# Kernel tuning notes

Hardware: AMD Instinct MI355X
Metric: run time of the kernel (lower is better)

Reference implementation:

```python
import jax, jax.numpy as jnp
import numpy as np

N_NODES = 50000
N_EDGES = 800000
IN_DIM = 64
OUT_DIM = 64
EDGE_DIM = 16
LN_EPS = 1e-5


def setup_inputs() -> dict:
    key = jax.random.key(0)
    ks = jax.random.split(key, 12)
    def lin(k, fan_in, fan_out):
        # torch nn.Linear default init: U(-1/sqrt(fan_in), 1/sqrt(fan_in))
        kw, kb = jax.random.split(k)
        bound = 1.0 / np.sqrt(fan_in)
        W = jax.random.uniform(kw, (fan_in, fan_out), jnp.float32, -bound, bound)
        b = jax.random.uniform(kb, (fan_out,), jnp.float32, -bound, bound)
        return W, b
    x = jax.random.normal(ks[0], (N_NODES, IN_DIM), jnp.float32)
    edge_index = jax.random.randint(ks[1], (2, N_EDGES), 0, N_NODES, jnp.int64 if jax.config.jax_enable_x64 else jnp.int32)
    edge_features = jax.random.normal(ks[2], (N_EDGES, EDGE_DIM), jnp.float32)
    W1, b1 = lin(ks[3], IN_DIM + EDGE_DIM, OUT_DIM)   # msg_mlp layer 1
    W2, b2 = lin(ks[4], OUT_DIM, OUT_DIM)             # msg_mlp layer 2
    W3, b3 = lin(ks[5], IN_DIM + OUT_DIM, OUT_DIM)    # update_mlp
    gamma = jnp.ones((OUT_DIM,), jnp.float32)
    beta = jnp.zeros((OUT_DIM,), jnp.float32)
    return {"x": x, "edge_index": edge_index, "edge_features": edge_features,
            "W1": W1, "b1": b1, "W2": W2, "b2": b2, "W3": W3, "b3": b3,
            "gamma": gamma, "beta": beta}


def reference(x, edge_index, edge_features, W1, b1, W2, b2, W3, b3, gamma, beta):
    num_nodes = x.shape[0]
    src, dst = edge_index[0], edge_index[1]
    # gather source node feats, concat with edge feats -> message MLP
    msg_in = jnp.concatenate([x[src], edge_features], axis=-1)           # [E, in+edge]
    h = jax.nn.relu(msg_in @ W1 + b1)
    messages = h @ W2 + b2                                               # [E, out]
    # scatter-add aggregate + mean by in-degree (count + 1e-8)
    agg = jax.ops.segment_sum(messages, dst, num_segments=num_nodes)     # [N, out]
    cnt = jax.ops.segment_sum(jnp.ones((messages.shape[0],), x.dtype), dst,
                              num_segments=num_nodes)[:, None]           # [N, 1]
    agg = agg / (cnt + 1e-8)
    # update MLP + residual (Identity since in_dim == out_dim) + LayerNorm
    updated = jax.nn.relu(jnp.concatenate([x, agg], axis=-1) @ W3 + b3)  # [N, out]
    y = updated + x
    mu = jnp.mean(y, axis=-1, keepdims=True)
    var = jnp.var(y, axis=-1, keepdims=True)
    return (y - mu) * jax.lax.rsqrt(var + LN_EPS) * gamma + beta
```

## Files before the change

### kernel.cpp

```cpp
#include <hip/hip_runtime.h>

typedef unsigned short u16;
typedef unsigned int u32;
typedef short short8 __attribute__((ext_vector_type(8)));
typedef short short4v __attribute__((ext_vector_type(4)));
typedef float floatx4 __attribute__((ext_vector_type(4)));

#define NE 800000
#define NNODES 50000
#define NBLK 196

#define EDGE_GRID 1536

#define LDS_FENCE() __asm__ volatile("s_waitcnt lgkmcnt(0)" ::: "memory")

__device__ __forceinline__ u16 f2bf(float f) {
    u32 r;
    asm("v_cvt_pk_bf16_f32 %0, %1, %2" : "=v"(r) : "v"(f), "v"(f));
    return (u16)r;
}
__device__ __forceinline__ u32 f2bf2(float lo, float hi) {
    u32 r;
    asm("v_cvt_pk_bf16_f32 %0, %1, %2" : "=v"(r) : "v"(lo), "v"(hi));
    return r;
}
__device__ __forceinline__ float bf2f(u16 u) {
    union { unsigned int i; float f; } v; v.i = ((unsigned int)u) << 16; return v.f;
}
__device__ __forceinline__ short8 pack8(const float4 a, const float4 b) {
    union { short8 s; u32 u[4]; } o;
    o.u[0] = f2bf2(a.x, a.y);
    o.u[1] = f2bf2(a.z, a.w);
    o.u[2] = f2bf2(b.x, b.y);
    o.u[3] = f2bf2(b.z, b.w);
    return o.s;
}
__device__ __forceinline__ short8 ld8_bf(const float* __restrict__ p) {
    return pack8(*(const float4*)p, *(const float4*)(p + 4));
}

#define MFMA16(a, b, c) __builtin_amdgcn_mfma_f32_16x16x32_bf16(a, b, c, 0, 0, 0)

__global__ __launch_bounds__(256) void prep_kernel(
    const float* __restrict__ x, const int* __restrict__ ei,
    int* __restrict__ hist, u16* __restrict__ xbf, float* __restrict__ agg)
{
    const int id = blockIdx.x * 256 + threadIdx.x;
    if (id < NE) {
        atomicAdd(&hist[ei[NE + id]], 1);
        float4 z; z.x = 0.f; z.y = 0.f; z.z = 0.f; z.w = 0.f;
        *(float4*)&agg[(size_t)id * 4] = z;
    }
    if (id < NNODES * 8) {
        *(short8*)&xbf[(size_t)id * 8] = ld8_bf(x + (size_t)id * 8);
    }
}

__global__ __launch_bounds__(256) void scan1_kernel(
    const int* __restrict__ hist, int* __restrict__ cursor, int* __restrict__ bsum)
{
    const int i = blockIdx.x * 256 + threadIdx.x;
    const int lane = threadIdx.x & 63;
    const int w = threadIdx.x >> 6;
    const int v = (i < NNODES) ? hist[i] : 0;
    int inc = v;
    #pragma unroll
    for (int o = 1; o < 64; o <<= 1) {
        const int tt = __shfl_up(inc, o);
        if (lane >= o) inc += tt;
    }
    __shared__ int ws[4];
    if (lane == 63) ws[w] = inc;
    __syncthreads();
    int add = 0;
    for (int j = 0; j < w; ++j) add += ws[j];
    const int excl = inc - v + add;
    if (i < NNODES) cursor[i] = excl;
    if (threadIdx.x == 255) bsum[blockIdx.x] = excl + v;
}

__global__ __launch_bounds__(256) void scatter_kernel(
    const int* __restrict__ ei, int* __restrict__ cursor,
    const int* __restrict__ bsum, uint2* __restrict__ sde)
{
    __shared__ int bsx[256];
    __shared__ int ws[4];
    {
        const int tid = threadIdx.x;
        const int lane = tid & 63;
        const int w = tid >> 6;
        const int v = (tid < NBLK) ? bsum[tid] : 0;
        int inc = v;
        #pragma unroll
        for (int o = 1; o < 64; o <<= 1) {
            const int tt = __shfl_up(inc, o);
            if (lane >= o) inc += tt;
        }
        if (lane == 63) ws[w] = inc;
        __syncthreads();
        int add = 0;
        for (int j = 0; j < w; ++j) add += ws[j];
        bsx[tid] = inc - v + add;
    }
    __syncthreads();

    const int e = blockIdx.x * 256 + threadIdx.x;
    if (e < NE) {
        const int dst = ei[NE + e];
        const int p = atomicAdd(&cursor[dst], 1) + bsx[dst >> 8];
        uint2 v;
        v.x = (u32)e;
        v.y = ((u32)ei[e] << 16) | (u32)dst;
        sde[p] = v;
    }
}

__global__ __launch_bounds__(256) void edge_kernel(
    const u16* __restrict__ xbf, const float* __restrict__ ef,
    const float* __restrict__ w1, const float* __restrict__ b1,
    const float* __restrict__ w2, const float* __restrict__ b2,
    const uint2* __restrict__ sde, float* __restrict__ agg)
{
    constexpr int S1 = 104;
    __shared__ u16 A1[4][16 * S1];
    __shared__ int Ds[4][16];
    __shared__ u16 W2f[2][4][64 * 8];

    const int wid  = threadIdx.x >> 6;
    const int lane = threadIdx.x & 63;
    const int q    = lane >> 4;
    const int c    = lane & 15;
    const int r4   = lane >> 2;
    const int p4   = lane & 3;

    short8 w1f[3][4];
    #pragma unroll
    for (int kk = 0; kk < 3; ++kk)
        #pragma unroll
        for (int nn = 0; nn < 4; ++nn)
            #pragma unroll
            for (int j = 0; j < 8; ++j) {
                const int k = kk * 32 + q * 8 + j;
                w1f[kk][nn][j] = (k < 80) ? (short)f2bf(w1[k * 64 + nn * 16 + c]) : (short)0;
            }
    if (wid == 0) {
        #pragma unroll
        for (int kk = 0; kk < 2; ++kk)
            #pragma unroll
            for (int nn = 0; nn < 4; ++nn) {
                short8 f;
                #pragma unroll
                for (int j = 0; j < 8; ++j) {
                    const int k = kk * 32 + q * 8 + j;
                    f[j] = (short)f2bf(w2[k * 64 + nn * 16 + c]);
                }
                *(short8*)&W2f[kk][nn][lane * 8] = f;
            }
    }
    float b1v[4], b2v[4];
    #pragma unroll
    for (int nn = 0; nn < 4; ++nn) {
        b1v[nn] = b1[nn * 16 + c];
        b2v[nn] = b2[nn * 16 + c];
    }
    if (q == 1) {
        const short8 z8 = {0, 0, 0, 0, 0, 0, 0, 0};
        *(short8*)&A1[wid][c * S1 + 80] = z8;
        *(short8*)&A1[wid][c * S1 + 88] = z8;
    }
    __syncthreads();

    const floatx4 zero = {0.f, 0.f, 0.f, 0.f};
    const int ntile = NE / 16;
    const int stride = gridDim.x * 4;
    int t = blockIdx.x * 4 + wid;

    uint2 sdB; u32 eB;
    short8 xa, xb; float4 ev;
    int dcur;
    {
        const uint2 sdA = sde[t * 16 + c];
        const u32  eA  = sde[t * 16 + r4].x;
        dcur = (int)(sdA.y & 0xffffu);
        const int sA = (int)(sdA.y >> 16);
        int tb = t + stride; if (tb >= ntile) tb = ntile - 1;
        sdB = sde[tb * 16 + c];
        eB  = sde[tb * 16 + r4].x;
        const u16* xp = xbf + (size_t)sA * 64 + q * 16;
        xa = *(const short8*)xp;
        xb = *(const short8*)(xp + 8);
        ev = *(const float4*)(ef + (size_t)eA * 16 + p4 * 4);
    }

    for (; t < ntile; t += stride) {
        u16* arow = &A1[wid][c * S1 + q * 16];
        *(short8*)arow       = xa;
        *(short8*)(arow + 8) = xb;
        {
            union { short4v s; u32 u[2]; } e4;
            e4.u[0] = f2bf2(ev.x, ev.y);
            e4.u[1] = f2bf2(ev.z, ev.w);
            *(short4v*)&A1[wid][r4 * S1 + 64 + p4 * 4] = e4.s;
        }
        if (q == 0) Ds[wid][c] = dcur;
        LDS_FENCE();

        short8 a1k[3];
        #pragma unroll
        for (int kk = 0; kk < 3; ++kk)
            a1k[kk] = *(const short8*)&A1[wid][c * S1 + kk * 32 + q * 8];

        const int dnext = (int)(sdB.y & 0xffffu);
        {
            const int sN = (int)(sdB.y >> 16);
            const u16* xp = xbf + (size_t)sN * 64 + q * 16;
            xa = *(const short8*)xp;
            xb = *(const short8*)(xp + 8);
            ev = *(const float4*)(ef + (size_t)eB * 16 + p4 * 4);
        }
        {
            int tb = t + 2 * stride; if (tb >= ntile) tb = ntile - 1;
            sdB = sde[tb * 16 + c];
            eB  = sde[tb * 16 + r4].x;
        }

        #pragma unroll
        for (int nn = 0; nn < 4; ++nn) {
            floatx4 acc = MFMA16(a1k[0], w1f[0][nn], zero);
            acc = MFMA16(a1k[1], w1f[1][nn], acc);
            acc = MFMA16(a1k[2], w1f[2][nn], acc);
            #pragma unroll
            for (int r = 0; r < 4; ++r) {
                const float h = fmaxf(acc[r] + b1v[nn], 0.f);
                A1[wid][(q * 4 + r) * S1 + nn * 16 + c] = f2bf(h);
            }
        }
        LDS_FENCE();

        short8 a2k[2];
        #pragma unroll
        for (int kk = 0; kk < 2; ++kk)
            a2k[kk] = *(const short8*)&A1[wid][c * S1 + kk * 32 + q * 8];

        #pragma unroll
        for (int nn = 0; nn < 4; ++nn) {
            const short8 wf0 = *(const short8*)&W2f[0][nn][lane * 8];
            const short8 wf1 = *(const short8*)&W2f[1][nn][lane * 8];
            floatx4 mg = MFMA16(a2k[0], wf0, zero);
            mg = MFMA16(a2k[1], wf1, mg);
            #pragma unroll
            for (int r = 0; r < 4; ++r)
                A1[wid][(q * 4 + r) * S1 + nn * 16 + c] = f2bf(mg[r] + b2v[nn]);
        }
        LDS_FENCE();

        int dc = Ds[wid][0];
        float acc = bf2f(A1[wid][lane]);
        #pragma unroll
        for (int row = 1; row < 16; ++row) {
            const int d = Ds[wid][row];
            const float v = bf2f(A1[wid][row * S1 + lane]);
            if (d == dc) {
                acc += v;
            } else {
                atomicAdd(&agg[(size_t)dc * 64 + lane], acc);
                dc = d;
                acc = v;
            }
        }
        atomicAdd(&agg[(size_t)dc * 64 + lane], acc);

        LDS_FENCE();

        dcur = dnext;
    }
}

__global__ __launch_bounds__(256) void node_kernel(
    const u16* __restrict__ xbf, const float* __restrict__ w3,
    const float* __restrict__ b3, const float* __restrict__ g,
    const float* __restrict__ bb, const float* __restrict__ agg,
    const int* __restrict__ hist, float* __restrict__ out)
{
    constexpr int S3 = 136;
    __shared__ u16 Cs[4][16 * S3];

    const int wid  = threadIdx.x >> 6;
    const int lane = threadIdx.x & 63;
    const int q    = lane >> 4;
    const int c    = lane & 15;

    short8 w3f[4][4];
    #pragma unroll
    for (int kk = 0; kk < 4; ++kk)
        #pragma unroll
        for (int nn = 0; nn < 4; ++nn)
            #pragma unroll
            for (int j = 0; j < 8; ++j) {
                const int k = kk * 32 + q * 8 + j;
                w3f[kk][nn][j] = (short)f2bf(w3[k * 64 + nn * 16 + c]);
            }
    float b3v[4], gv[4], bv[4];
    #pragma unroll
    for (int nn = 0; nn < 4; ++nn) {
        b3v[nn] = b3[nn * 16 + c];
        gv[nn]  = g[nn * 16 + c];
        bv[nn]  = bb[nn * 16 + c];
    }

    const floatx4 zero = {0.f, 0.f, 0.f, 0.f};
    const int ntile = NNODES / 16;

    for (int t = blockIdx.x * 4 + wid; t < ntile; t += gridDim.x * 4) {
        const int n0 = t * 16;
        const int node = n0 + c;
        u16* crow = &Cs[wid][c * S3];

        if (q < 2) {
            const u16* xp = xbf + (size_t)node * 64 + q * 32;
            *(short8*)&crow[q * 32]      = *(const short8*)xp;
            *(short8*)&crow[q * 32 + 8]  = *(const short8*)(xp + 8);
            *(short8*)&crow[q * 32 + 16] = *(const short8*)(xp + 16);
            *(short8*)&crow[q * 32 + 24] = *(const short8*)(xp + 24);
        } else {
            const int p = q - 2;
            const float inv = 1.0f / ((float)hist[node] + 1e-8f);
            const float* ap = agg + (size_t)node * 64 + p * 32;
            #pragma unroll
            for (int gi = 0; gi < 4; ++gi) {
                const float4 v0 = *(const float4*)(ap + gi * 8);
                const float4 v1 = *(const float4*)(ap + gi * 8 + 4);
                union { short8 s; u32 u[4]; } o;
                o.u[0] = f2bf2(v0.x * inv, v0.y * inv);
                o.u[1] = f2bf2(v0.z * inv, v0.w * inv);
                o.u[2] = f2bf2(v1.x * inv, v1.y * inv);
                o.u[3] = f2bf2(v1.z * inv, v1.w * inv);
                *(short8*)&crow[64 + p * 32 + gi * 8] = o.s;
            }
        }
        LDS_FENCE();

        short8 af[4];
        #pragma unroll
        for (int kk = 0; kk < 4; ++kk)
            af[kk] = *(const short8*)&Cs[wid][c * S3 + kk * 32 + q * 8];

        float y[4][4];
        float s[4]  = {0.f, 0.f, 0.f, 0.f};
        float ss[4] = {0.f, 0.f, 0.f, 0.f};
        #pragma unroll
        for (int nn = 0; nn < 4; ++nn) {
            floatx4 acc = MFMA16(af[0], w3f[0][nn], zero);
            acc = MFMA16(af[1], w3f[1][nn], acc);
            acc = MFMA16(af[2], w3f[2][nn], acc);
            acc = MFMA16(af[3], w3f[3][nn], acc);
            #pragma unroll
            for (int r = 0; r < 4; ++r) {
                const float upd = fmaxf(acc[r] + b3v[nn], 0.f);
                const float xv = bf2f(Cs[wid][(q * 4 + r) * S3 + nn * 16 + c]);
                const float yy = upd + xv;
                y[r][nn] = yy;
                s[r] += yy;
                ss[r] += yy * yy;
            }
        }

        #pragma unroll
        for (int r = 0; r < 4; ++r) {
            float sr = s[r], sq = ss[r];
            #pragma unroll
            for (int off = 1; off < 16; off <<= 1) {
                sr += __shfl_xor(sr, off);
                sq += __shfl_xor(sq, off);
            }
            const float mu  = sr * (1.0f / 64.0f);
            const float var = sq * (1.0f / 64.0f) - mu * mu;
            const float rs  = rsqrtf(var + 1e-5f);
            float* op = out + (size_t)(n0 + q * 4 + r) * 64 + c;
            #pragma unroll
            for (int nn = 0; nn < 4; ++nn)
                op[nn * 16] = (y[r][nn] - mu) * rs * gv[nn] + bv[nn];
        }
    }
}

extern "C" void kernel_launch(void* const* d_in, const int* in_sizes, int n_in,
                              void* d_out, int out_size, void* d_ws, size_t ws_size,
                              hipStream_t stream) {
    const float* x   = (const float*)d_in[0];
    const int*   ei  = (const int*)d_in[1];
    const float* ef  = (const float*)d_in[2];
    const float* w1  = (const float*)d_in[3];
    const float* b1  = (const float*)d_in[4];
    const float* w2  = (const float*)d_in[5];
    const float* b2  = (const float*)d_in[6];
    const float* w3  = (const float*)d_in[7];
    const float* b3  = (const float*)d_in[8];
    const float* g   = (const float*)d_in[9];
    const float* bb  = (const float*)d_in[10];

    float* agg   = (float*)d_ws;
    int* hist    = (int*)d_ws + 3200000;
    int* cursor  = hist + NNODES;
    int* bsum    = cursor + NNODES;
    int* bsumx   = bsum + 256;
    u16* xbf     = (u16*)(bsumx + 256);
    uint2* sde   = (uint2*)((int*)d_ws + 4900512);

    hipMemsetAsync(hist, 0, (size_t)NNODES * sizeof(int), stream);
    prep_kernel<<<3125, 256, 0, stream>>>(x, ei, hist, xbf, agg);
    scan1_kernel<<<NBLK, 256, 0, stream>>>(hist, cursor, bsum);
    scatter_kernel<<<3125, 256, 0, stream>>>(ei, cursor, bsum, sde);
    edge_kernel<<<EDGE_GRID, 256, 0, stream>>>(xbf, ef, w1, b1, w2, b2, sde, agg);
    node_kernel<<<782, 256, 0, stream>>>(xbf, w3, b3, g, bb, agg, hist, (float*)d_out);
}
```

Before: 274.7 us.

## Use atomic work counter for dynamic edge-tile scheduling across waves

Replaces the static grid-stride assignment of 16-edge tiles in the edge kernel with a global atomic counter. Each wave claims its next tile one iteration ahead, which is meant to balance uneven tile costs such as atomic scatter runs. The memset is widened so the counter starts at zero. The bf16 conversion also moves from the packed hardware instruction to a software round-to-nearest-even, and the edge-feature packing now uses the scalar helper. The costs are one extra same-address atomic per tile per wave, which can contend across all waves, and more ALU work per conversion.

```diff
diff --git a/kernel.cpp b/kernel.cpp
--- a/kernel.cpp
+++ b/kernel.cpp
@@ -15,9 +15,8 @@
 #define LDS_FENCE() __asm__ volatile("s_waitcnt lgkmcnt(0)" ::: "memory")
 
 __device__ __forceinline__ u16 f2bf(float f) {
-    u32 r;
-    asm("v_cvt_pk_bf16_f32 %0, %1, %2" : "=v"(r) : "v"(f), "v"(f));
-    return (u16)r;
+    union { float f; unsigned int i; } v; v.f = f;
+    return (u16)((v.i + 0x7fffu + ((v.i >> 16) & 1u)) >> 16);
 }
 __device__ __forceinline__ u32 f2bf2(float lo, float hi) {
     u32 r;
@@ -119,7 +118,8 @@
     const u16* __restrict__ xbf, const float* __restrict__ ef,
     const float* __restrict__ w1, const float* __restrict__ b1,
     const float* __restrict__ w2, const float* __restrict__ b2,
-    const uint2* __restrict__ sde, float* __restrict__ agg)
+    const uint2* __restrict__ sde, float* __restrict__ agg,
+    int* __restrict__ ctr)
 {
     constexpr int S1 = 104;
     __shared__ u16 A1[4][16 * S1];
@@ -172,18 +172,28 @@
 
     const floatx4 zero = {0.f, 0.f, 0.f, 0.f};
     const int ntile = NE / 16;
-    const int stride = gridDim.x * 4;
-    int t = blockIdx.x * 4 + wid;
+
+    int t_cur, t_nxt;
+    {
+        int v0 = 0, v1 = 0;
+        if (lane == 0) {
+            v0 = atomicAdd(ctr, 1);
+            v1 = atomicAdd(ctr, 1);
+        }
+        t_cur = __shfl(v0, 0);
+        t_nxt = __shfl(v1, 0);
+    }
 
     uint2 sdB; u32 eB;
     short8 xa, xb; float4 ev;
     int dcur;
     {
-        const uint2 sdA = sde[t * 16 + c];
-        const u32  eA  = sde[t * 16 + r4].x;
+        const int ta = (t_cur < ntile) ? t_cur : (ntile - 1);
+        const uint2 sdA = sde[ta * 16 + c];
+        const u32  eA  = sde[ta * 16 + r4].x;
         dcur = (int)(sdA.y & 0xffffu);
         const int sA = (int)(sdA.y >> 16);
-        int tb = t + stride; if (tb >= ntile) tb = ntile - 1;
+        const int tb = (t_nxt < ntile) ? t_nxt : (ntile - 1);
         sdB = sde[tb * 16 + c];
         eB  = sde[tb * 16 + r4].x;
         const u16* xp = xbf + (size_t)sA * 64 + q * 16;
@@ -192,15 +202,15 @@
         ev = *(const float4*)(ef + (size_t)eA * 16 + p4 * 4);
     }
 
-    for (; t < ntile; t += stride) {
+    while (t_cur < ntile) {
         u16* arow = &A1[wid][c * S1 + q * 16];
         *(short8*)arow       = xa;
         *(short8*)(arow + 8) = xb;
         {
-            union { short4v s; u32 u[2]; } e4;
-            e4.u[0] = f2bf2(ev.x, ev.y);
-            e4.u[1] = f2bf2(ev.z, ev.w);
-            *(short4v*)&A1[wid][r4 * S1 + 64 + p4 * 4] = e4.s;
+            short4v e4;
+            e4[0] = (short)f2bf(ev.x); e4[1] = (short)f2bf(ev.y);
+            e4[2] = (short)f2bf(ev.z); e4[3] = (short)f2bf(ev.w);
+            *(short4v*)&A1[wid][r4 * S1 + 64 + p4 * 4] = e4;
         }
         if (q == 0) Ds[wid][c] = dcur;
         LDS_FENCE();
@@ -209,6 +219,13 @@
         #pragma unroll
         for (int kk = 0; kk < 3; ++kk)
             a1k[kk] = *(const short8*)&A1[wid][c * S1 + kk * 32 + q * 8];
+
+        int t_new;
+        {
+            int v = 0;
+            if (lane == 0) v = atomicAdd(ctr, 1);
+            t_new = __shfl(v, 0);
+        }
 
         const int dnext = (int)(sdB.y & 0xffffu);
         {
@@ -219,7 +236,7 @@
             ev = *(const float4*)(ef + (size_t)eB * 16 + p4 * 4);
         }
         {
-            int tb = t + 2 * stride; if (tb >= ntile) tb = ntile - 1;
+            const int tb = (t_new < ntile) ? t_new : (ntile - 1);
             sdB = sde[tb * 16 + c];
             eB  = sde[tb * 16 + r4].x;
         }
@@ -273,6 +290,8 @@
         LDS_FENCE();
 
         dcur = dnext;
+        t_cur = t_nxt;
+        t_nxt = t_new;
     }
 }
 
@@ -406,11 +425,12 @@
     int* bsumx   = bsum + 256;
     u16* xbf     = (u16*)(bsumx + 256);
     uint2* sde   = (uint2*)((int*)d_ws + 4900512);
-
-    hipMemsetAsync(hist, 0, (size_t)NNODES * sizeof(int), stream);
+    int* ctr     = bsumx;
+
+    hipMemsetAsync(hist, 0, (size_t)(NNODES + NNODES + 256 + 256) * sizeof(int), stream);
     prep_kernel<<<3125, 256, 0, stream>>>(x, ei, hist, xbf, agg);
     scan1_kernel<<<NBLK, 256, 0, stream>>>(hist, cursor, bsum);
     scatter_kernel<<<3125, 256, 0, stream>>>(ei, cursor, bsum, sde);
-    edge_kernel<<<EDGE_GRID, 256, 0, stream>>>(xbf, ef, w1, b1, w2, b2, sde, agg);
+    edge_kernel<<<EDGE_GRID, 256, 0, stream>>>(xbf, ef, w1, b1, w2, b2, sde, agg, ctr);
     node_kernel<<<782, 256, 0, stream>>>(xbf, w3, b3, g, bb, agg, hist, (float*)d_out);
 }
```

Result: slower. 939.4 us (+242.0%).
